# Kernel tuning notes

Measured on AMD Instinct MI355X. Metric: run time of the kernel, lower is better.

Reference implementation:

```python
import jax, jax.numpy as jnp
import numpy as np

LN_EPS = 1e-5


def layer_norm(x, gamma, beta):
    mu = jnp.mean(x, axis=-1, keepdims=True)
    var = jnp.mean(jnp.square(x - mu), axis=-1, keepdims=True)
    return (x - mu) * jax.lax.rsqrt(var + LN_EPS) * gamma + beta


def setup_inputs() -> dict:
    key = jax.random.key(0)
    ks = jax.random.split(key, 7)
    B, S, D = 8, 1024, 512
    H, Dh = 8, 64
    scale = 1.0 / np.sqrt(D)
    x = jax.random.normal(ks[0], (B, S, D), dtype=jnp.float32)
    Wq = jax.random.normal(ks[1], (D, H * Dh), dtype=jnp.float32) * scale
    Wk = jax.random.normal(ks[2], (D, H * Dh), dtype=jnp.float32) * scale
    Wv = jax.random.normal(ks[3], (D, H * Dh), dtype=jnp.float32) * scale
    Wfc = jax.random.normal(ks[4], (H * Dh, D), dtype=jnp.float32) * scale
    gamma = jnp.ones((D,), dtype=jnp.float32)
    beta = jnp.zeros((D,), dtype=jnp.float32)
    return {"x": x, "Wq": Wq, "Wk": Wk, "Wv": Wv, "Wfc": Wfc, "gamma": gamma, "beta": beta}


def reference(x, Wq, Wk, Wv, Wfc, gamma, beta):
    B, S, D = x.shape
    H, Dh = 8, 64
    Q = (x @ Wq).reshape(B, S, H, Dh).transpose(0, 2, 1, 3)  # [B,H,S,Dh]
    K = (x @ Wk).reshape(B, S, H, Dh).transpose(0, 2, 1, 3)
    V = (x @ Wv).reshape(B, S, H, Dh).transpose(0, 2, 1, 3)
    scores = jnp.einsum('bhqd,bhkd->bhqk', Q, K) / np.sqrt(Dh).astype(np.float32)
    # tridiagonal band mask; NOTE: original fills off-band with -1e-09 (not -inf)
    idx = jnp.arange(S)
    band = jnp.abs(idx[:, None] - idx[None, :]) <= 1  # [S,S]
    scores = jnp.where(band, scores, jnp.float32(-1e-09))
    attn = jax.nn.softmax(scores, axis=-1)
    context = jnp.einsum('bhqk,bhkd->bhqd', attn, V)  # [B,H,S,Dh]
    context = context.transpose(0, 2, 1, 3).reshape(B, S, H * Dh)
    out = context @ Wfc
    return layer_norm(out + x, gamma, beta)
```

## Files before the change

kernel.cpp:

```cpp
#include <hip/hip_runtime.h>
#include <math.h>


typedef short     s8v  __attribute__((ext_vector_type(8)));
typedef float     f4v  __attribute__((ext_vector_type(4)));
typedef unsigned short us4v __attribute__((ext_vector_type(4)));
typedef unsigned short us8v __attribute__((ext_vector_type(8)));

__device__ __forceinline__ unsigned short f2b(float f) {
  union { float f; unsigned int u; } v; v.f = f;
  unsigned int u = v.u;
  return (unsigned short)((u + 0x7fffu + ((u >> 16) & 1u)) >> 16);
}
__device__ __forceinline__ float b2f(unsigned short u) {
  union { unsigned int i; float f; } v; v.i = ((unsigned int)u) << 16;
  return v.f;
}
__device__ __forceinline__ void gload_lds16(const void* g, void* l) {
  __builtin_amdgcn_global_load_lds(
      (const __attribute__((address_space(1))) void*)g,
      (__attribute__((address_space(3))) void*)l, 16, 0, 0);
}

__global__ __launch_bounds__(256) void conv_kernel(
    const float* __restrict__ x,
    const float* __restrict__ Wq, const float* __restrict__ Wk,
    const float* __restrict__ Wv, const float* __restrict__ Wfc,
    unsigned short* __restrict__ xb, unsigned short* __restrict__ Wt,
    float* __restrict__ Vsum) {
  __shared__ unsigned short tile[32][33];
  const int bid = blockIdx.x, t = threadIdx.x;
  if (bid < 4096) {
    const int i = bid * 256 + t;
    const float4 f = ((const float4*)x)[i];
    us4v o; o[0] = f2b(f.x); o[1] = f2b(f.y); o[2] = f2b(f.z); o[3] = f2b(f.w);
    ((us4v*)xb)[i] = o;
  } else if (bid < 5120) {
    const int id = bid - 4096;
    const int z = id >> 8, rem = id & 255;
    const int bx = rem & 15, by = rem >> 4;
    const float* W = (z == 0) ? Wq : (z == 1) ? Wk : (z == 2) ? Wv : Wfc;
    const int tx = t & 31, ty = t >> 5;
    const int n0 = bx * 32, k0 = by * 32;
    #pragma unroll
    for (int r = ty; r < 32; r += 8)
      tile[r][tx] = f2b(W[(size_t)(k0 + r) * 512 + n0 + tx]);
    __syncthreads();
    unsigned short* dst = Wt + (size_t)z * 512 * 512;
    #pragma unroll
    for (int r = ty; r < 32; r += 8)
      dst[(size_t)(n0 + r) * 512 + k0 + tx] = tile[tx][r];
  } else {
    float4 zz = {0.f, 0.f, 0.f, 0.f};
    #pragma unroll
    for (int p = 0; p < 4; ++p) ((float4*)Vsum)[p * 256 + t] = zz;
  }
}

__global__ __launch_bounds__(256) void gemm_qkv_kernel(
    const unsigned short* __restrict__ A, const unsigned short* __restrict__ Bt,
    unsigned short* __restrict__ C, float* __restrict__ Vsum) {
  const int N = 1536, K = 512;
  __shared__ __align__(16) unsigned short smem[16384];
  unsigned short* As = smem;
  unsigned short* Bs = smem + 8192;
  const int t = threadIdx.x, wave = t >> 6, lane = t & 63;
  const int wr = wave >> 1, wc = wave & 1;
  const int quad = lane >> 4, l16 = lane & 15;
  const int bm = blockIdx.y * 128, bn = blockIdx.x * 128;

  const unsigned short *gA[4], *gB[4];
  #pragma unroll
  for (int p = 0; p < 4; ++p) {
    const int ci = wave * 256 + p * 64 + lane;
    const int r = ci >> 3, c = (ci & 7) ^ (r & 7);
    gA[p] = A + (size_t)(bm + r) * K + c * 8;
    gB[p] = Bt + (size_t)(bn + r) * K + c * 8;
  }

  f4v acc[4][4];
  #pragma unroll
  for (int i = 0; i < 4; ++i)
    #pragma unroll
    for (int j = 0; j < 4; ++j) {
      f4v z = {0.f, 0.f, 0.f, 0.f};
      acc[i][j] = z;
    }

  for (int kt = 0; kt < K; kt += 64) {
    #pragma unroll
    for (int p = 0; p < 4; ++p)
      gload_lds16(gA[p] + kt, As + wave * 2048 + p * 512);
    #pragma unroll
    for (int p = 0; p < 4; ++p)
      gload_lds16(gB[p] + kt, Bs + wave * 2048 + p * 512);
    __syncthreads();

    #pragma unroll
    for (int s = 0; s < 2; ++s) {
      s8v af[4], bf[4];
      #pragma unroll
      for (int i = 0; i < 4; ++i) {
        const int r = wr * 64 + i * 16 + l16;
        af[i] = *(const s8v*)&As[(r * 8 + ((quad + 4 * s) ^ (r & 7))) * 8];
      }
      #pragma unroll
      for (int j = 0; j < 4; ++j) {
        const int r = wc * 64 + j * 16 + l16;
        bf[j] = *(const s8v*)&Bs[(r * 8 + ((quad + 4 * s) ^ (r & 7))) * 8];
      }
      #pragma unroll
      for (int i = 0; i < 4; ++i)
        #pragma unroll
        for (int j = 0; j < 4; ++j)
          acc[i][j] = __builtin_amdgcn_mfma_f32_16x16x32_bf16(
              af[i], bf[j], acc[i][j], 0, 0, 0);
    }
    __syncthreads();
  }

  if (bn >= 1024) {
    const int b = bm >> 10;
    #pragma unroll
    for (int j = 0; j < 4; ++j) {
      float ps = 0.f;
      #pragma unroll
      for (int i = 0; i < 4; ++i)
        #pragma unroll
        for (int r = 0; r < 4; ++r) ps += acc[i][j][r];
      ps += __shfl_xor(ps, 16);
      ps += __shfl_xor(ps, 32);
      if (quad == 0)
        atomicAdd(&Vsum[b * 512 + (bn - 1024) + wc * 64 + j * 16 + l16], ps);
    }
  }

  #pragma unroll
  for (int i = 0; i < 4; ++i) {
    const int lr0 = wr * 64 + i * 16 + quad * 4;
    #pragma unroll
    for (int j = 0; j < 4; ++j) {
      const int lc = wc * 64 + j * 16 + l16;
      #pragma unroll
      for (int r = 0; r < 4; ++r)
        smem[(lr0 + r) * 128 + lc] = f2b(acc[i][j][r]);
    }
  }
  __syncthreads();
  #pragma unroll
  for (int p = 0; p < 8; ++p) {
    const int row = p * 16 + (t >> 4);
    const int ch  = t & 15;
    *(us8v*)(C + (size_t)(bm + row) * N + bn + ch * 8) =
        *(const us8v*)&smem[row * 128 + ch * 8];
  }
}

#define KVS 68
__global__ __launch_bounds__(256) void attn_kernel(
    const unsigned short* __restrict__ QKV, const float* __restrict__ Vsum,
    unsigned short* __restrict__ ctx) {
  __shared__ __align__(16) unsigned short Qs[130 * KVS];
  __shared__ __align__(16) unsigned short Ks[130 * KVS];
  __shared__ __align__(16) unsigned short Vs[130 * KVS];
  __shared__ __align__(16) float vs_s[64];
  const int bh = blockIdx.x;
  const int b = bh >> 3, h = bh & 7;
  const int q0 = blockIdx.y * 128;
  const int t = threadIdx.x;
  const size_t rowb = ((size_t)b * 1024) * 1536;

  #pragma unroll
  for (int p = 0; p < 5; ++p) {
    const int i = p * 32 + (t >> 3);
    if (i < 130) {
      int g = q0 - 1 + i;
      g = g < 0 ? 0 : (g > 1023 ? 1023 : g);
      const unsigned short* src =
          QKV + rowb + (size_t)g * 1536 + h * 64 + (t & 7) * 8;
      const us8v qv = *(const us8v*)(src);
      const us8v kv = *(const us8v*)(src + 512);
      const us8v vv = *(const us8v*)(src + 1024);
      us4v lo, hi;
      #pragma unroll
      for (int r = 0; r < 4; ++r) { lo[r] = qv[r]; hi[r] = qv[r + 4]; }
      *(us4v*)&Qs[i * KVS + (t & 7) * 8]     = lo;
      *(us4v*)&Qs[i * KVS + (t & 7) * 8 + 4] = hi;
      #pragma unroll
      for (int r = 0; r < 4; ++r) { lo[r] = kv[r]; hi[r] = kv[r + 4]; }
      *(us4v*)&Ks[i * KVS + (t & 7) * 8]     = lo;
      *(us4v*)&Ks[i * KVS + (t & 7) * 8 + 4] = hi;
      #pragma unroll
      for (int r = 0; r < 4; ++r) { lo[r] = vv[r]; hi[r] = vv[r + 4]; }
      *(us4v*)&Vs[i * KVS + (t & 7) * 8]     = lo;
      *(us4v*)&Vs[i * KVS + (t & 7) * 8 + 4] = hi;
    }
  }
  if (t < 64) vs_s[t] = Vsum[(b << 9) + h * 64 + t];
  __syncthreads();

  const int q    = q0 + (t >> 1);
  const int half = t & 1;
  const int li   = (t >> 1) + 1;
  const int co   = half * 32;

  float pm = 0.f, p0 = 0.f, pp = 0.f;
  #pragma unroll
  for (int jj = 0; jj < 8; ++jj) {
    const us4v qv = *(const us4v*)&Qs[li * KVS + co + jj * 4];
    const us4v km = *(const us4v*)&Ks[(li - 1) * KVS + co + jj * 4];
    const us4v k0 = *(const us4v*)&Ks[li * KVS + co + jj * 4];
    const us4v kp = *(const us4v*)&Ks[(li + 1) * KVS + co + jj * 4];
    #pragma unroll
    for (int r = 0; r < 4; ++r) {
      const float qf = b2f(qv[r]);
      pm += qf * b2f(km[r]);
      p0 += qf * b2f(k0[r]);
      pp += qf * b2f(kp[r]);
    }
  }
  pm += __shfl_xor(pm, 1);
  p0 += __shfl_xor(p0, 1);
  pp += __shfl_xor(pp, 1);

  const float OFF = -1e-9f;
  const float s0 = p0 * 0.125f;
  const float sm = (q > 0)    ? pm * 0.125f : OFF;
  const float sp = (q < 1023) ? pp * 0.125f : OFF;
  const float m  = fmaxf(fmaxf(s0, sm), fmaxf(sp, OFF));
  const float e0 = __expf(s0 - m), em = __expf(sm - m), ep = __expf(sp - m);
  const float eoff = __expf(OFF - m);
  const float inv  = 1.f / (e0 + em + ep + 1021.f * eoff);
  const float wm = (em - eoff) * inv, w0 = (e0 - eoff) * inv,
              wp = (ep - eoff) * inv, wt = eoff * inv;

  unsigned short* cp = ctx + ((size_t)(b * 1024 + q)) * 512 + h * 64 + co;
  #pragma unroll
  for (int jj = 0; jj < 8; ++jj) {
    const us4v a  = *(const us4v*)&Vs[(li - 1) * KVS + co + jj * 4];
    const us4v v0 = *(const us4v*)&Vs[li * KVS + co + jj * 4];
    const us4v c  = *(const us4v*)&Vs[(li + 1) * KVS + co + jj * 4];
    const float4 vsv = *(const float4*)&vs_s[co + jj * 4];
    us4v o;
    o[0] = f2b(wt * vsv.x + wm * b2f(a[0]) + w0 * b2f(v0[0]) + wp * b2f(c[0]));
    o[1] = f2b(wt * vsv.y + wm * b2f(a[1]) + w0 * b2f(v0[1]) + wp * b2f(c[1]));
    o[2] = f2b(wt * vsv.z + wm * b2f(a[2]) + w0 * b2f(v0[2]) + wp * b2f(c[2]));
    o[3] = f2b(wt * vsv.w + wm * b2f(a[3]) + w0 * b2f(v0[3]) + wp * b2f(c[3]));
    *(us4v*)(cp + jj * 4) = o;
  }
}

#define OS 516

__global__ __launch_bounds__(512) void gemm_fcln_kernel(
    const unsigned short* __restrict__ A,
    const unsigned short* __restrict__ Bt,
    const unsigned short* __restrict__ xb, const float* __restrict__ gamma,
    const float* __restrict__ beta, float* __restrict__ y) {
  const int K = 512;
  __shared__ __align__(16) unsigned short smem[69632];
  float* outS = (float*)smem;

  const int t = threadIdx.x, wave = t >> 6, lane = t & 63;
  const int wrr = wave >> 2, wcc = wave & 3;
  const int quad = lane >> 4, l16 = lane & 15;
  const int bm = blockIdx.x * 32;

  const int ciA = wave * 64 + lane;
  const int rA = ciA >> 3, cA = (ciA & 7) ^ (rA & 7);
  const unsigned short* gA = A + (size_t)(bm + rA) * K + cA * 8;
  const unsigned short* gB[8];
  #pragma unroll
  for (int p = 0; p < 8; ++p) {
    const int ci = wave * 512 + p * 64 + lane;
    const int r = ci >> 3, c = (ci & 7) ^ (r & 7);
    gB[p] = Bt + (size_t)r * K + c * 8;
  }

  f4v acc[8];
  #pragma unroll
  for (int j = 0; j < 8; ++j) {
    f4v z = {0.f, 0.f, 0.f, 0.f};
    acc[j] = z;
  }

  if (wave < 4) gload_lds16(gA, smem + wave * 512);
  #pragma unroll
  for (int p = 0; p < 8; ++p)
    gload_lds16(gB[p], smem + 2048 + wave * 4096 + p * 512);
  __syncthreads();

  for (int it = 0; it < 8; ++it) {
    const int cur = (it & 1) * 34816;
    const int nxt = 34816 - cur;
    const unsigned short* Ab = smem + cur;
    const unsigned short* Bb = smem + cur + 2048;
    const int rm = wrr * 16 + l16;
    const s8v af0 = *(const s8v*)&Ab[(rm * 8 + (quad ^ (rm & 7))) * 8];
    const s8v af1 = *(const s8v*)&Ab[(rm * 8 + ((quad + 4) ^ (rm & 7))) * 8];
    s8v bf0[8];
    #pragma unroll
    for (int j = 0; j < 8; ++j) {
      const int n = wcc * 128 + j * 16 + l16;
      bf0[j] = *(const s8v*)&Bb[(n * 8 + (quad ^ (n & 7))) * 8];
    }
    if (it < 7) {
      const int kt = (it + 1) * 64;
      if (wave < 4) gload_lds16(gA + kt, smem + nxt + wave * 512);
      #pragma unroll
      for (int p = 0; p < 8; ++p)
        gload_lds16(gB[p] + kt, smem + nxt + 2048 + wave * 4096 + p * 512);
    }
    #pragma unroll
    for (int j = 0; j < 8; ++j)
      acc[j] = __builtin_amdgcn_mfma_f32_16x16x32_bf16(af0, bf0[j], acc[j], 0, 0, 0);
    #pragma unroll
    for (int j = 0; j < 8; ++j) {
      const int n = wcc * 128 + j * 16 + l16;
      const s8v bf1 = *(const s8v*)&Bb[(n * 8 + ((quad + 4) ^ (n & 7))) * 8];
      acc[j] = __builtin_amdgcn_mfma_f32_16x16x32_bf16(af1, bf1, acc[j], 0, 0, 0);
    }
    __syncthreads();
  }

  #pragma unroll
  for (int j = 0; j < 8; ++j) {
    const int col = wcc * 128 + j * 16 + l16;
    const int row0 = wrr * 16 + quad * 4;
    #pragma unroll
    for (int r = 0; r < 4; ++r)
      outS[(row0 + r) * OS + col] = acc[j][r];
  }
  __syncthreads();

  const int row = t >> 4, l = t & 15;
  const size_t gbase = (size_t)(bm + row) * 512;
  float4 v[8];
  float s1 = 0.f, s2 = 0.f;
  #pragma unroll
  for (int k = 0; k < 8; ++k) {
    const int c = k * 64 + l * 4;
    const float4 a = *(const float4*)&outS[row * OS + c];
    const us4v xv = *(const us4v*)&xb[gbase + c];
    float4 w;
    w.x = a.x + b2f(xv[0]); w.y = a.y + b2f(xv[1]);
    w.z = a.z + b2f(xv[2]); w.w = a.w + b2f(xv[3]);
    v[k] = w;
    s1 += w.x + w.y + w.z + w.w;
    s2 += w.x * w.x + w.y * w.y + w.z * w.z + w.w * w.w;
  }
  #pragma unroll
  for (int m = 1; m < 16; m <<= 1) {
    s1 += __shfl_xor(s1, m);
    s2 += __shfl_xor(s2, m);
  }
  const float mu  = s1 * (1.f / 512.f);
  const float var = s2 * (1.f / 512.f) - mu * mu;
  const float rs  = rsqrtf(var + 1e-5f);
  #pragma unroll
  for (int k = 0; k < 8; ++k) {
    const int c = k * 64 + l * 4;
    const float4 g  = *(const float4*)&gamma[c];
    const float4 bb = *(const float4*)&beta[c];
    float4 o;
    o.x = (v[k].x - mu) * rs * g.x + bb.x;
    o.y = (v[k].y - mu) * rs * g.y + bb.y;
    o.z = (v[k].z - mu) * rs * g.z + bb.z;
    o.w = (v[k].w - mu) * rs * g.w + bb.w;
    *(float4*)&y[gbase + c] = o;
  }
}

extern "C" void kernel_launch(void* const* d_in, const int* in_sizes, int n_in,
                              void* d_out, int out_size, void* d_ws, size_t ws_size,
                              hipStream_t stream) {
  const float* x     = (const float*)d_in[0];
  const float* Wq    = (const float*)d_in[1];
  const float* Wk    = (const float*)d_in[2];
  const float* Wv    = (const float*)d_in[3];
  const float* Wfc   = (const float*)d_in[4];
  const float* gamma = (const float*)d_in[5];
  const float* beta  = (const float*)d_in[6];
  float* y = (float*)d_out;

  char* ws = (char*)d_ws;
  unsigned short* Wt   = (unsigned short*)(ws);
  unsigned short* xb   = (unsigned short*)(ws + 2097152);
  unsigned short* QKV  = (unsigned short*)(ws + 10485760);
  float*          Vsum = (float*)(ws + 35651584);
  unsigned short* ctx  = (unsigned short*)(ws + 35667968);

  conv_kernel<<<5121, 256, 0, stream>>>(x, Wq, Wk, Wv, Wfc, xb, Wt, Vsum);
  gemm_qkv_kernel<<<dim3(12, 64), 256, 0, stream>>>(xb, Wt, QKV, Vsum);
  attn_kernel<<<dim3(64, 8), 256, 0, stream>>>(QKV, Vsum, ctx);
  gemm_fcln_kernel<<<256, 512, 0, stream>>>(
      ctx, Wt + (size_t)1536 * 512, xb, gamma, beta, y);
}
```

Measured before the change: 128.1 us.

## Fuse banded attention into FC+LayerNorm kernel and enlarge QKV GEMM tile

Merges the attention kernel into the FC GEMM + LayerNorm kernel. Each block now computes the context for 32 query rows across all heads straight into LDS and feeds it as the A operand of the FC GEMM, so the ctx buffer never goes through global memory and one launch disappears. The QKV GEMM moves to 512 threads with 256x128 tiles, halving the block count and raising reuse of the B tile. The price is redundant K/V halo loads per chunk, a longer serial prologue before the GEMM in the fused kernel, and more LDS per block, which may lower occupancy.

```diff
diff --git a/kernel.cpp b/kernel.cpp
--- a/kernel.cpp
+++ b/kernel.cpp
@@ -57,24 +57,29 @@
   }
 }
 
-__global__ __launch_bounds__(256) void gemm_qkv_kernel(
+__global__ __launch_bounds__(512) void gemm_qkv_kernel(
     const unsigned short* __restrict__ A, const unsigned short* __restrict__ Bt,
     unsigned short* __restrict__ C, float* __restrict__ Vsum) {
   const int N = 1536, K = 512;
-  __shared__ __align__(16) unsigned short smem[16384];
+  __shared__ __align__(16) unsigned short smem[24576];
   unsigned short* As = smem;
-  unsigned short* Bs = smem + 8192;
+  unsigned short* Bs = smem + 16384;
   const int t = threadIdx.x, wave = t >> 6, lane = t & 63;
   const int wr = wave >> 1, wc = wave & 1;
   const int quad = lane >> 4, l16 = lane & 15;
-  const int bm = blockIdx.y * 128, bn = blockIdx.x * 128;
-
-  const unsigned short *gA[4], *gB[4];
+  const int bm = blockIdx.y * 256, bn = blockIdx.x * 128;
+
+  const unsigned short *gA[4], *gB[2];
   #pragma unroll
   for (int p = 0; p < 4; ++p) {
     const int ci = wave * 256 + p * 64 + lane;
     const int r = ci >> 3, c = (ci & 7) ^ (r & 7);
     gA[p] = A + (size_t)(bm + r) * K + c * 8;
+  }
+  #pragma unroll
+  for (int p = 0; p < 2; ++p) {
+    const int ci = wave * 128 + p * 64 + lane;
+    const int r = ci >> 3, c = (ci & 7) ^ (r & 7);
     gB[p] = Bt + (size_t)(bn + r) * K + c * 8;
   }
 
@@ -92,8 +97,8 @@
     for (int p = 0; p < 4; ++p)
       gload_lds16(gA[p] + kt, As + wave * 2048 + p * 512);
     #pragma unroll
-    for (int p = 0; p < 4; ++p)
-      gload_lds16(gB[p] + kt, Bs + wave * 2048 + p * 512);
+    for (int p = 0; p < 2; ++p)
+      gload_lds16(gB[p] + kt, Bs + wave * 1024 + p * 512);
     __syncthreads();
 
     #pragma unroll
@@ -120,7 +125,7 @@
   }
 
   if (bn >= 1024) {
-    const int b = bm >> 10;
+    const int b = blockIdx.y >> 2;
     #pragma unroll
     for (int j = 0; j < 4; ++j) {
       float ps = 0.f;
@@ -136,145 +141,137 @@
   }
 
   #pragma unroll
-  for (int i = 0; i < 4; ++i) {
-    const int lr0 = wr * 64 + i * 16 + quad * 4;
-    #pragma unroll
-    for (int j = 0; j < 4; ++j) {
-      const int lc = wc * 64 + j * 16 + l16;
-      #pragma unroll
-      for (int r = 0; r < 4; ++r)
-        smem[(lr0 + r) * 128 + lc] = f2b(acc[i][j][r]);
-    }
-  }
-  __syncthreads();
-  #pragma unroll
-  for (int p = 0; p < 8; ++p) {
-    const int row = p * 16 + (t >> 4);
-    const int ch  = t & 15;
-    *(us8v*)(C + (size_t)(bm + row) * N + bn + ch * 8) =
-        *(const us8v*)&smem[row * 128 + ch * 8];
-  }
-}
-
-#define KVS 68
-__global__ __launch_bounds__(256) void attn_kernel(
+  for (int h2 = 0; h2 < 2; ++h2) {
+    if ((wr >> 1) == h2) {
+      #pragma unroll
+      for (int i = 0; i < 4; ++i) {
+        const int lr0 = (wr & 1) * 64 + i * 16 + quad * 4;
+        #pragma unroll
+        for (int j = 0; j < 4; ++j) {
+          const int lc = wc * 64 + j * 16 + l16;
+          #pragma unroll
+          for (int r = 0; r < 4; ++r)
+            smem[(lr0 + r) * 128 + lc] = f2b(acc[i][j][r]);
+        }
+      }
+    }
+    __syncthreads();
+    #pragma unroll
+    for (int p = 0; p < 4; ++p) {
+      const int row = p * 32 + (t >> 4);
+      const int ch  = t & 15;
+      *(us8v*)(C + (size_t)(bm + h2 * 128 + row) * N + bn + ch * 8) =
+          *(const us8v*)&smem[row * 128 + ch * 8];
+    }
+    __syncthreads();
+  }
+}
+
+#define KS 520
+#define CTXO 0
+#define VSO  16384
+#define WKO  17408
+__global__ __launch_bounds__(512) void attn_fcln_kernel(
     const unsigned short* __restrict__ QKV, const float* __restrict__ Vsum,
-    unsigned short* __restrict__ ctx) {
-  __shared__ __align__(16) unsigned short Qs[130 * KVS];
-  __shared__ __align__(16) unsigned short Ks[130 * KVS];
-  __shared__ __align__(16) unsigned short Vs[130 * KVS];
-  __shared__ __align__(16) float vs_s[64];
-  const int bh = blockIdx.x;
-  const int b = bh >> 3, h = bh & 7;
-  const int q0 = blockIdx.y * 128;
-  const int t = threadIdx.x;
-  const size_t rowb = ((size_t)b * 1024) * 1536;
-
-  #pragma unroll
-  for (int p = 0; p < 5; ++p) {
-    const int i = p * 32 + (t >> 3);
-    if (i < 130) {
-      int g = q0 - 1 + i;
-      g = g < 0 ? 0 : (g > 1023 ? 1023 : g);
-      const unsigned short* src =
-          QKV + rowb + (size_t)g * 1536 + h * 64 + (t & 7) * 8;
-      const us8v qv = *(const us8v*)(src);
-      const us8v kv = *(const us8v*)(src + 512);
-      const us8v vv = *(const us8v*)(src + 1024);
-      us4v lo, hi;
-      #pragma unroll
-      for (int r = 0; r < 4; ++r) { lo[r] = qv[r]; hi[r] = qv[r + 4]; }
-      *(us4v*)&Qs[i * KVS + (t & 7) * 8]     = lo;
-      *(us4v*)&Qs[i * KVS + (t & 7) * 8 + 4] = hi;
-      #pragma unroll
-      for (int r = 0; r < 4; ++r) { lo[r] = kv[r]; hi[r] = kv[r + 4]; }
-      *(us4v*)&Ks[i * KVS + (t & 7) * 8]     = lo;
-      *(us4v*)&Ks[i * KVS + (t & 7) * 8 + 4] = hi;
-      #pragma unroll
-      for (int r = 0; r < 4; ++r) { lo[r] = vv[r]; hi[r] = vv[r + 4]; }
-      *(us4v*)&Vs[i * KVS + (t & 7) * 8]     = lo;
-      *(us4v*)&Vs[i * KVS + (t & 7) * 8 + 4] = hi;
-    }
-  }
-  if (t < 64) vs_s[t] = Vsum[(b << 9) + h * 64 + t];
-  __syncthreads();
-
-  const int q    = q0 + (t >> 1);
-  const int half = t & 1;
-  const int li   = (t >> 1) + 1;
-  const int co   = half * 32;
-
-  float pm = 0.f, p0 = 0.f, pp = 0.f;
-  #pragma unroll
-  for (int jj = 0; jj < 8; ++jj) {
-    const us4v qv = *(const us4v*)&Qs[li * KVS + co + jj * 4];
-    const us4v km = *(const us4v*)&Ks[(li - 1) * KVS + co + jj * 4];
-    const us4v k0 = *(const us4v*)&Ks[li * KVS + co + jj * 4];
-    const us4v kp = *(const us4v*)&Ks[(li + 1) * KVS + co + jj * 4];
-    #pragma unroll
-    for (int r = 0; r < 4; ++r) {
-      const float qf = b2f(qv[r]);
-      pm += qf * b2f(km[r]);
-      p0 += qf * b2f(k0[r]);
-      pp += qf * b2f(kp[r]);
-    }
-  }
-  pm += __shfl_xor(pm, 1);
-  p0 += __shfl_xor(p0, 1);
-  pp += __shfl_xor(pp, 1);
-
-  const float OFF = -1e-9f;
-  const float s0 = p0 * 0.125f;
-  const float sm = (q > 0)    ? pm * 0.125f : OFF;
-  const float sp = (q < 1023) ? pp * 0.125f : OFF;
-  const float m  = fmaxf(fmaxf(s0, sm), fmaxf(sp, OFF));
-  const float e0 = __expf(s0 - m), em = __expf(sm - m), ep = __expf(sp - m);
-  const float eoff = __expf(OFF - m);
-  const float inv  = 1.f / (e0 + em + ep + 1021.f * eoff);
-  const float wm = (em - eoff) * inv, w0 = (e0 - eoff) * inv,
-              wp = (ep - eoff) * inv, wt = eoff * inv;
-
-  unsigned short* cp = ctx + ((size_t)(b * 1024 + q)) * 512 + h * 64 + co;
-  #pragma unroll
-  for (int jj = 0; jj < 8; ++jj) {
-    const us4v a  = *(const us4v*)&Vs[(li - 1) * KVS + co + jj * 4];
-    const us4v v0 = *(const us4v*)&Vs[li * KVS + co + jj * 4];
-    const us4v c  = *(const us4v*)&Vs[(li + 1) * KVS + co + jj * 4];
-    const float4 vsv = *(const float4*)&vs_s[co + jj * 4];
-    us4v o;
-    o[0] = f2b(wt * vsv.x + wm * b2f(a[0]) + w0 * b2f(v0[0]) + wp * b2f(c[0]));
-    o[1] = f2b(wt * vsv.y + wm * b2f(a[1]) + w0 * b2f(v0[1]) + wp * b2f(c[1]));
-    o[2] = f2b(wt * vsv.z + wm * b2f(a[2]) + w0 * b2f(v0[2]) + wp * b2f(c[2]));
-    o[3] = f2b(wt * vsv.w + wm * b2f(a[3]) + w0 * b2f(v0[3]) + wp * b2f(c[3]));
-    *(us4v*)(cp + jj * 4) = o;
-  }
-}
-
-#define OS 516
-
-__global__ __launch_bounds__(512) void gemm_fcln_kernel(
-    const unsigned short* __restrict__ A,
     const unsigned short* __restrict__ Bt,
     const unsigned short* __restrict__ xb, const float* __restrict__ gamma,
     const float* __restrict__ beta, float* __restrict__ y) {
-  const int K = 512;
-  __shared__ __align__(16) unsigned short smem[69632];
-  float* outS = (float*)smem;
+  __shared__ __align__(16) unsigned short smem[69408];
+  unsigned short* ctxS = smem + CTXO;
+  float* vs = (float*)(smem + VSO);
+  unsigned short* WK = smem + WKO;
+  unsigned short* Qs = WK;
+  unsigned short* Ks = WK + 16640;
+  unsigned short* Vs = WK + 34320;
 
   const int t = threadIdx.x, wave = t >> 6, lane = t & 63;
+  const int quad = lane >> 4, l16 = lane & 15;
+  const int b = blockIdx.x >> 5, chunk = blockIdx.x & 31;
+  const int q0 = chunk * 32;
+  const size_t rowb = ((size_t)b * 1024) * 1536;
+
+  for (int i = t; i < 6400; i += 512) {
+    int row, ch, off;
+    unsigned short* dst;
+    if (i < 2048) { row = i >> 6; ch = i & 63; off = 0;
+                    dst = Qs + row * KS + ch * 8; row = q0 + row; }
+    else if (i < 4224) { int k = i - 2048; row = k >> 6; ch = k & 63; off = 512;
+                    dst = Ks + (k >> 6) * KS + ch * 8;
+                    row = q0 - 1 + row; row = row < 0 ? 0 : (row > 1023 ? 1023 : row); }
+    else { int k = i - 4224; row = k >> 6; ch = k & 63; off = 1024;
+                    dst = Vs + (k >> 6) * KS + ch * 8;
+                    row = q0 - 1 + row; row = row < 0 ? 0 : (row > 1023 ? 1023 : row); }
+    *(us8v*)dst = *(const us8v*)(QKV + rowb + (size_t)row * 1536 + off + ch * 8);
+  }
+  vs[t] = Vsum[b * 512 + t];
+  __syncthreads();
+
+  {
+    const int pair = t >> 1, half = t & 1;
+    const int qr = pair & 31, h = pair >> 5;
+    const int q = q0 + qr;
+    const int colb = h * 64 + half * 32;
+    float pm = 0.f, p0 = 0.f, pp = 0.f;
+    #pragma unroll
+    for (int jj = 0; jj < 4; ++jj) {
+      const us8v qv = *(const us8v*)&Qs[qr * KS + colb + jj * 8];
+      const us8v km = *(const us8v*)&Ks[qr * KS + colb + jj * 8];
+      const us8v k0 = *(const us8v*)&Ks[(qr + 1) * KS + colb + jj * 8];
+      const us8v kp = *(const us8v*)&Ks[(qr + 2) * KS + colb + jj * 8];
+      #pragma unroll
+      for (int r = 0; r < 8; ++r) {
+        const float qf = b2f(qv[r]);
+        pm += qf * b2f(km[r]);
+        p0 += qf * b2f(k0[r]);
+        pp += qf * b2f(kp[r]);
+      }
+    }
+    pm += __shfl_xor(pm, 1);
+    p0 += __shfl_xor(p0, 1);
+    pp += __shfl_xor(pp, 1);
+
+    const float OFF = -1e-9f;
+    const float s0 = p0 * 0.125f;
+    const float sm = (q > 0)    ? pm * 0.125f : OFF;
+    const float sp = (q < 1023) ? pp * 0.125f : OFF;
+    const float m  = fmaxf(fmaxf(s0, sm), fmaxf(sp, OFF));
+    const float e0 = __expf(s0 - m), em = __expf(sm - m), ep = __expf(sp - m);
+    const float eoff = __expf(OFF - m);
+    const float inv  = 1.f / (e0 + em + ep + 1021.f * eoff);
+    const float wm = (em - eoff) * inv, w0 = (e0 - eoff) * inv,
+                wp = (ep - eoff) * inv, wt = eoff * inv;
+
+    #pragma unroll
+    for (int jj = 0; jj < 4; ++jj) {
+      const us8v a  = *(const us8v*)&Vs[qr * KS + colb + jj * 8];
+      const us8v v0 = *(const us8v*)&Vs[(qr + 1) * KS + colb + jj * 8];
+      const us8v c  = *(const us8v*)&Vs[(qr + 2) * KS + colb + jj * 8];
+      const float4 va = *(const float4*)&vs[colb + jj * 8];
+      const float4 vb = *(const float4*)&vs[colb + jj * 8 + 4];
+      us8v o;
+      #pragma unroll
+      for (int r = 0; r < 4; ++r) {
+        const float base = (r == 0) ? va.x : (r == 1) ? va.y : (r == 2) ? va.z : va.w;
+        o[r] = f2b(wt * base + wm * b2f(a[r]) + w0 * b2f(v0[r]) + wp * b2f(c[r]));
+      }
+      #pragma unroll
+      for (int r = 4; r < 8; ++r) {
+        const float base = (r == 4) ? vb.x : (r == 5) ? vb.y : (r == 6) ? vb.z : vb.w;
+        o[r] = f2b(wt * base + wm * b2f(a[r]) + w0 * b2f(v0[r]) + wp * b2f(c[r]));
+      }
+      const int slot = h * 8 + ((half * 4 + jj) ^ (qr & 7));
+      *(us8v*)&ctxS[qr * 512 + slot * 8] = o;
+    }
+  }
+  __syncthreads();
+
   const int wrr = wave >> 2, wcc = wave & 3;
-  const int quad = lane >> 4, l16 = lane & 15;
-  const int bm = blockIdx.x * 32;
-
-  const int ciA = wave * 64 + lane;
-  const int rA = ciA >> 3, cA = (ciA & 7) ^ (rA & 7);
-  const unsigned short* gA = A + (size_t)(bm + rA) * K + cA * 8;
-  const unsigned short* gB[8];
-  #pragma unroll
-  for (int p = 0; p < 8; ++p) {
-    const int ci = wave * 512 + p * 64 + lane;
-    const int r = ci >> 3, c = (ci & 7) ^ (r & 7);
-    gB[p] = Bt + (size_t)r * K + c * 8;
+  const unsigned short* gB[4];
+  #pragma unroll
+  for (int p = 0; p < 4; ++p) {
+    const int ci = wave * 256 + p * 64 + lane;
+    const int R = ci >> 3, pos = (ci & 7) ^ (R & 7);
+    gB[p] = Bt + (size_t)(2 * R + (pos >> 2)) * 512 + (pos & 3) * 8;
   }
 
   f4v acc[8];
@@ -284,63 +281,56 @@
     acc[j] = z;
   }
 
-  if (wave < 4) gload_lds16(gA, smem + wave * 512);
-  #pragma unroll
-  for (int p = 0; p < 8; ++p)
-    gload_lds16(gB[p], smem + 2048 + wave * 4096 + p * 512);
+  #pragma unroll
+  for (int p = 0; p < 4; ++p)
+    gload_lds16(gB[p], WK + wave * 2048 + p * 512);
   __syncthreads();
 
-  for (int it = 0; it < 8; ++it) {
-    const int cur = (it & 1) * 34816;
-    const int nxt = 34816 - cur;
-    const unsigned short* Ab = smem + cur;
-    const unsigned short* Bb = smem + cur + 2048;
+  for (int it = 0; it < 16; ++it) {
+    const unsigned short* Bb = WK + (it & 1) * 16384;
     const int rm = wrr * 16 + l16;
-    const s8v af0 = *(const s8v*)&Ab[(rm * 8 + (quad ^ (rm & 7))) * 8];
-    const s8v af1 = *(const s8v*)&Ab[(rm * 8 + ((quad + 4) ^ (rm & 7))) * 8];
-    s8v bf0[8];
+    const int c = it * 4 + quad;
+    const int slot = (c & ~7) | ((c & 7) ^ (rm & 7));
+    const s8v af = *(const s8v*)&ctxS[rm * 512 + slot * 8];
+    s8v bf[8];
     #pragma unroll
     for (int j = 0; j < 8; ++j) {
       const int n = wcc * 128 + j * 16 + l16;
-      bf0[j] = *(const s8v*)&Bb[(n * 8 + (quad ^ (n & 7))) * 8];
-    }
-    if (it < 7) {
-      const int kt = (it + 1) * 64;
-      if (wave < 4) gload_lds16(gA + kt, smem + nxt + wave * 512);
-      #pragma unroll
-      for (int p = 0; p < 8; ++p)
-        gload_lds16(gB[p] + kt, smem + nxt + 2048 + wave * 4096 + p * 512);
+      bf[j] = *(const s8v*)&Bb[(n >> 1) * 64 +
+                               ((((n & 1) * 4 + quad) ^ ((n >> 1) & 7)) * 8)];
+    }
+    if (it < 15) {
+      const int kt = (it + 1) * 32;
+      unsigned short* nb = WK + ((it & 1) ^ 1) * 16384 + wave * 2048;
+      #pragma unroll
+      for (int p = 0; p < 4; ++p)
+        gload_lds16(gB[p] + kt, nb + p * 512);
     }
     #pragma unroll
     for (int j = 0; j < 8; ++j)
-      acc[j] = __builtin_amdgcn_mfma_f32_16x16x32_bf16(af0, bf0[j], acc[j], 0, 0, 0);
-    #pragma unroll
-    for (int j = 0; j < 8; ++j) {
-      const int n = wcc * 128 + j * 16 + l16;
-      const s8v bf1 = *(const s8v*)&Bb[(n * 8 + ((quad + 4) ^ (n & 7))) * 8];
-      acc[j] = __builtin_amdgcn_mfma_f32_16x16x32_bf16(af1, bf1, acc[j], 0, 0, 0);
-    }
-    __syncthreads();
-  }
-
+      acc[j] = __builtin_amdgcn_mfma_f32_16x16x32_bf16(af, bf[j], acc[j], 0, 0, 0);
+    __syncthreads();
+  }
+
+  float* outS = (float*)WK;
   #pragma unroll
   for (int j = 0; j < 8; ++j) {
     const int col = wcc * 128 + j * 16 + l16;
     const int row0 = wrr * 16 + quad * 4;
     #pragma unroll
     for (int r = 0; r < 4; ++r)
-      outS[(row0 + r) * OS + col] = acc[j][r];
+      outS[(row0 + r) * 516 + col] = acc[j][r];
   }
   __syncthreads();
 
   const int row = t >> 4, l = t & 15;
-  const size_t gbase = (size_t)(bm + row) * 512;
+  const size_t gbase = ((size_t)(b * 1024 + q0 + row)) * 512;
   float4 v[8];
   float s1 = 0.f, s2 = 0.f;
   #pragma unroll
   for (int k = 0; k < 8; ++k) {
     const int c = k * 64 + l * 4;
-    const float4 a = *(const float4*)&outS[row * OS + c];
+    const float4 a = *(const float4*)&outS[row * 516 + c];
     const us4v xv = *(const us4v*)&xb[gbase + c];
     float4 w;
     w.x = a.x + b2f(xv[0]); w.y = a.y + b2f(xv[1]);
@@ -388,11 +378,9 @@
   unsigned short* xb   = (unsigned short*)(ws + 2097152);
   unsigned short* QKV  = (unsigned short*)(ws + 10485760);
   float*          Vsum = (float*)(ws + 35651584);
-  unsigned short* ctx  = (unsigned short*)(ws + 35667968);
 
   conv_kernel<<<5121, 256, 0, stream>>>(x, Wq, Wk, Wv, Wfc, xb, Wt, Vsum);
-  gemm_qkv_kernel<<<dim3(12, 64), 256, 0, stream>>>(xb, Wt, QKV, Vsum);
-  attn_kernel<<<dim3(64, 8), 256, 0, stream>>>(QKV, Vsum, ctx);
-  gemm_fcln_kernel<<<256, 512, 0, stream>>>(
-      ctx, Wt + (size_t)1536 * 512, xb, gamma, beta, y);
-}
+  gemm_qkv_kernel<<<dim3(12, 32), 512, 0, stream>>>(xb, Wt, QKV, Vsum);
+  attn_fcln_kernel<<<256, 512, 0, stream>>>(
+      QKV, Vsum, Wt + (size_t)1536 * 512, xb, gamma, beta, y);
+}
```

Result: slower. 135.8 us (+6.0%).

## Double-buffer QKV GEMM LDS tiles with K-step 32 and prefetch

Applied to the files above, without the earlier changes.

Restructures the QKV projection GEMM main loop from single-buffered 64-wide K tiles to double-buffered 32-wide K tiles. The next tile's global-to-LDS loads are issued before the MFMAs on the current tile, so memory latency can overlap compute, and the XOR swizzle is adapted to the 4-chunk row layout. It also fully unrolls the K loop in the second GEMM kernel. The cost is more iterations with one barrier each and larger unrolled code.

```diff
diff --git a/kernel.cpp b/kernel.cpp
--- a/kernel.cpp
+++ b/kernel.cpp
@@ -62,20 +62,19 @@
     unsigned short* __restrict__ C, float* __restrict__ Vsum) {
   const int N = 1536, K = 512;
   __shared__ __align__(16) unsigned short smem[16384];
-  unsigned short* As = smem;
-  unsigned short* Bs = smem + 8192;
   const int t = threadIdx.x, wave = t >> 6, lane = t & 63;
   const int wr = wave >> 1, wc = wave & 1;
   const int quad = lane >> 4, l16 = lane & 15;
   const int bm = blockIdx.y * 128, bn = blockIdx.x * 128;
-
-  const unsigned short *gA[4], *gB[4];
-  #pragma unroll
-  for (int p = 0; p < 4; ++p) {
-    const int ci = wave * 256 + p * 64 + lane;
-    const int r = ci >> 3, c = (ci & 7) ^ (r & 7);
-    gA[p] = A + (size_t)(bm + r) * K + c * 8;
-    gB[p] = Bt + (size_t)(bn + r) * K + c * 8;
+  const int sw = (l16 >> 1) & 3;
+
+  const unsigned short *gA[2], *gB[2];
+  #pragma unroll
+  for (int s = 0; s < 2; ++s) {
+    const int ci = wave * 128 + s * 64 + lane;
+    const int r = ci >> 2, c = (ci & 3) ^ ((r >> 1) & 3);
+    gA[s] = A + (size_t)(bm + r) * K + c * 8;
+    gB[s] = Bt + (size_t)(bn + r) * K + c * 8;
   }
 
   f4v acc[4][4];
@@ -87,35 +86,45 @@
       acc[i][j] = z;
     }
 
-  for (int kt = 0; kt < K; kt += 64) {
-    #pragma unroll
-    for (int p = 0; p < 4; ++p)
-      gload_lds16(gA[p] + kt, As + wave * 2048 + p * 512);
-    #pragma unroll
-    for (int p = 0; p < 4; ++p)
-      gload_lds16(gB[p] + kt, Bs + wave * 2048 + p * 512);
-    __syncthreads();
-
-    #pragma unroll
-    for (int s = 0; s < 2; ++s) {
-      s8v af[4], bf[4];
-      #pragma unroll
-      for (int i = 0; i < 4; ++i) {
-        const int r = wr * 64 + i * 16 + l16;
-        af[i] = *(const s8v*)&As[(r * 8 + ((quad + 4 * s) ^ (r & 7))) * 8];
+  #pragma unroll
+  for (int s = 0; s < 2; ++s) {
+    gload_lds16(gA[s], smem + wave * 1024 + s * 512);
+    gload_lds16(gB[s], smem + 4096 + wave * 1024 + s * 512);
+  }
+  __syncthreads();
+
+  #pragma unroll
+  for (int it = 0; it < 16; ++it) {
+    const int cur = (it & 1) * 8192;
+    const int nxt = 8192 - cur;
+    const unsigned short* As = smem + cur;
+    const unsigned short* Bs = smem + cur + 4096;
+
+    s8v af[4], bf[4];
+    #pragma unroll
+    for (int i = 0; i < 4; ++i) {
+      const int r = wr * 64 + i * 16 + l16;
+      af[i] = *(const s8v*)&As[(r * 4 + (quad ^ sw)) * 8];
+    }
+    #pragma unroll
+    for (int j = 0; j < 4; ++j) {
+      const int r = wc * 64 + j * 16 + l16;
+      bf[j] = *(const s8v*)&Bs[(r * 4 + (quad ^ sw)) * 8];
+    }
+    if (it < 15) {
+      const int kt = (it + 1) * 32;
+      #pragma unroll
+      for (int s = 0; s < 2; ++s) {
+        gload_lds16(gA[s] + kt, smem + nxt + wave * 1024 + s * 512);
+        gload_lds16(gB[s] + kt, smem + nxt + 4096 + wave * 1024 + s * 512);
       }
-      #pragma unroll
-      for (int j = 0; j < 4; ++j) {
-        const int r = wc * 64 + j * 16 + l16;
-        bf[j] = *(const s8v*)&Bs[(r * 8 + ((quad + 4 * s) ^ (r & 7))) * 8];
-      }
-      #pragma unroll
-      for (int i = 0; i < 4; ++i)
-        #pragma unroll
-        for (int j = 0; j < 4; ++j)
-          acc[i][j] = __builtin_amdgcn_mfma_f32_16x16x32_bf16(
-              af[i], bf[j], acc[i][j], 0, 0, 0);
-    }
+    }
+    #pragma unroll
+    for (int i = 0; i < 4; ++i)
+      #pragma unroll
+      for (int j = 0; j < 4; ++j)
+        acc[i][j] = __builtin_amdgcn_mfma_f32_16x16x32_bf16(
+            af[i], bf[j], acc[i][j], 0, 0, 0);
     __syncthreads();
   }
 
@@ -290,6 +299,7 @@
     gload_lds16(gB[p], smem + 2048 + wave * 4096 + p * 512);
   __syncthreads();
 
+  #pragma unroll
   for (int it = 0; it < 8; ++it) {
     const int cur = (it & 1) * 34816;
     const int nxt = 34816 - cur;
```

Result: faster. 123.6 us (-3.5%).
